# Kernel tuning notes

Measured on AMD Instinct MI355X. Metric: run time of the kernel, lower is better.

The kernel has to match this reference:

```python
import jax, jax.numpy as jnp
import numpy as np

NUM_EXPERTS = 8


def setup_inputs() -> dict:
    key = jax.random.key(0)
    k1, k2, k3, k4 = jax.random.split(key, 4)
    T, H, I, E = 1024, 1024, 4096, NUM_EXPERTS
    return {
        "hidden_states": jax.random.normal(k1, (T, H), dtype=jnp.float32),
        "w1": jax.random.normal(k2, (E, 2 * I, H), dtype=jnp.float32) * 0.02,
        "w2": jax.random.normal(k3, (E, H, I), dtype=jnp.float32) * 0.02,
        "gating_output": jax.random.normal(k4, (T, E), dtype=jnp.float32),
        "topk": 2,
    }


def reference(hidden_states, w1, w2, gating_output, topk):
    # Faithful single-device version of jax_fused_moe_func (renormalize=True,
    # reduce_results=True). The original sorts token copies by expert id and runs
    # a grouped matmul (megablox gmm), then reverts the sort; mathematically each
    # token copy is multiplied by its expert's weights, which we compute directly
    # (no sort/unsort permutation needed since it cancels).
    orig_shape = hidden_states.shape
    dtype = hidden_states.dtype
    H = hidden_states.shape[-1]
    T = hidden_states.size // H
    E = w1.shape[0]
    I = w2.shape[-1]  # intermediate_size

    hs = hidden_states.reshape(T, H)
    gates = gating_output.reshape(T, E)

    probs = jax.nn.softmax(gates.astype(jnp.float32), axis=-1)
    topk_weights, topk_indices = jax.lax.top_k(probs, k=topk)
    topk_weights = topk_weights / topk_weights.sum(axis=-1, keepdims=True)  # renormalize
    topk_weights = topk_weights.astype(dtype)

    flat_ids = topk_indices.reshape(-1)            # [T*topk] expert id per token copy
    x = jnp.repeat(hs, topk, axis=0)               # [T*topk, H] token copies

    out = jnp.zeros((T * topk, H), dtype=dtype)
    for e in range(E):  # fixed small expert loop (emulates grouped GEMM)
        h = x @ w1[e].T                            # [m, 2I]
        act = jax.nn.silu(h[:, :I]) * h[:, I:]     # SwiGLU
        y = act @ w2[e].T                          # [m, H]
        out = jnp.where((flat_ids == e)[:, None], y, out)

    out = (out.reshape(T, topk, H) * topk_weights[..., None]).sum(axis=-2)
    return out.reshape(orig_shape)
```

## Files before the change

kernel.cpp:

```cpp
#include <hip/hip_runtime.h>

#define T_TOK 1024
#define H_DIM 1024
#define I_DIM 4096
#define NE 8

typedef __attribute__((ext_vector_type(8))) short bf16x8;
typedef __attribute__((ext_vector_type(4))) float f32x4;
typedef __attribute__((ext_vector_type(8))) unsigned short us8;

__device__ __forceinline__ unsigned short f2bf(float x) {
  union { float f; unsigned u; } v; v.f = x;
  unsigned r = v.u + 0x7fffu + ((v.u >> 16) & 1u);
  return (unsigned short)(r >> 16);
}

__device__ __forceinline__ unsigned cvt_pk_bf16(float a, float b) {
  unsigned r;
  asm("v_cvt_pk_bf16_f32 %0, %1, %2" : "=v"(r) : "v"(a), "v"(b));
  return r;
}

__global__ void k_route(const float* __restrict__ gates, int* __restrict__ counts,
                        int* __restrict__ tok_idx, float* __restrict__ tok_w,
                        int* __restrict__ tok_cpy) {
  int t = blockIdx.x * blockDim.x + threadIdx.x;
  if (t >= T_TOK) return;
  float g[NE];
#pragma unroll
  for (int e = 0; e < NE; ++e) g[e] = gates[t * NE + e];
  int i1 = 0; float g1 = g[0];
#pragma unroll
  for (int e = 1; e < NE; ++e) if (g[e] > g1) { g1 = g[e]; i1 = e; }
  int i2 = -1; float g2 = -1e30f;
#pragma unroll
  for (int e = 0; e < NE; ++e) if (e != i1 && g[e] > g2) { g2 = g[e]; i2 = e; }
  float wa = 1.0f / (1.0f + expf(g2 - g1));
  float wb = 1.0f - wa;
  int s1 = atomicAdd(&counts[i1], 1);
  tok_idx[i1 * T_TOK + s1] = t; tok_w[i1 * T_TOK + s1] = wa; tok_cpy[i1 * T_TOK + s1] = 0;
  int s2 = atomicAdd(&counts[i2], 1);
  tok_idx[i2 * T_TOK + s2] = t; tok_w[i2 * T_TOK + s2] = wb; tok_cpy[i2 * T_TOK + s2] = 1;
}

__global__ void k_pack(const float* __restrict__ hs, const int* __restrict__ counts,
                       const int* __restrict__ tok_idx, const float* __restrict__ tok_w,
                       const int* __restrict__ tok_cpy, unsigned short* __restrict__ xpack,
                       int* __restrict__ row_tok, float* __restrict__ row_w,
                       int* __restrict__ inv_row) {
  int e = blockIdx.x >> 10, slot = blockIdx.x & 1023;
  if (slot >= counts[e]) return;
  int off = 0;
#pragma unroll
  for (int i = 0; i < NE; ++i) if (i < e) off += counts[i];
  int row = off + slot;
  int tok = tok_idx[e * T_TOK + slot];
  if (threadIdx.x == 0) {
    row_tok[row] = tok;
    row_w[row] = tok_w[e * T_TOK + slot];
    inv_row[tok * 2 + tok_cpy[e * T_TOK + slot]] = row;
  }
  float4 v = ((const float4*)(hs + (size_t)tok * H_DIM))[threadIdx.x];
  uint2 o; o.x = cvt_pk_bf16(v.x, v.y); o.y = cvt_pk_bf16(v.z, v.w);
  ((uint2*)(xpack + (size_t)row * H_DIM))[threadIdx.x] = o;
}

#define BK 64

__global__ __launch_bounds__(256)
void k_gemm1(const float* __restrict__ w1, const unsigned short* __restrict__ xpack,
             const int* __restrict__ counts, unsigned short* __restrict__ act) {
  int b = blockIdx.x;
  int x = b & 7, s = b >> 3;
  int mt = s & 7, pl = s >> 3;
  int panel = pl * 8 + x;
  int e = panel >> 6, ntile = panel & 63;
  int cnt = counts[e];
  int m0 = mt * 128;
  if (m0 >= cnt) return;
  int off = 0;
#pragma unroll
  for (int i = 0; i < NE; ++i) if (i < e) off += counts[i];
  int n0 = ntile * 64;

  __shared__ __align__(16) short As[128 * BK];
  __shared__ __align__(16) short Bs[128 * BK];

  int tid = threadIdx.x;
  int lane = tid & 63, wid = tid >> 6;
  int wm = wid & 1, wn = wid >> 1;
  int lr = lane & 15, lk8 = (lane >> 4) * 8;

  const float* w1e = w1 + (size_t)e * (2 * I_DIM) * H_DIM;
  const unsigned short* xb = xpack + (size_t)(off + m0) * H_DIM;

  int arow0 = tid >> 3, ack = tid & 7;
  int brow0 = tid >> 4, bck = tid & 15;

  const unsigned short* aptr[4];
  int awoff[4];
#pragma unroll
  for (int i = 0; i < 4; ++i) {
    int r = arow0 + i * 32;
    aptr[i] = xb + (size_t)r * H_DIM + ack * 8;
    awoff[i] = r * BK + ((ack * 8) ^ ((r & 7) << 3));
  }
  const float* bptr[8];
  int bwoff[8];
#pragma unroll
  for (int i = 0; i < 8; ++i) {
    int r = brow0 + i * 16;
    int grow = ((r & 16) ? I_DIM : 0) + n0 + ((r >> 5) << 4) + (r & 15);
    bptr[i] = w1e + (size_t)grow * H_DIM + bck * 4;
    bwoff[i] = r * BK + ((bck * 4) ^ ((r & 7) << 3));
  }

  f32x4 acc[4][4];
#pragma unroll
  for (int i = 0; i < 4; ++i)
#pragma unroll
    for (int j = 0; j < 4; ++j) acc[i][j] = (f32x4){0.f, 0.f, 0.f, 0.f};

  us8 aReg[4];
  float4 bReg[8];

  auto loadA = [&](int k0) {
#pragma unroll
    for (int i = 0; i < 4; ++i) {
      us8 z = {0, 0, 0, 0, 0, 0, 0, 0};
      aReg[i] = (m0 + arow0 + i * 32 < cnt) ? *(const us8*)(aptr[i] + k0) : z;
    }
  };
  auto loadB = [&](int k0) {
#pragma unroll
    for (int i = 0; i < 8; ++i) bReg[i] = *(const float4*)(bptr[i] + k0);
  };

  loadA(0); loadB(0);

  for (int ks = 0; ks < H_DIM / BK; ++ks) {
    __syncthreads();
#pragma unroll
    for (int i = 0; i < 4; ++i) *(us8*)&As[awoff[i]] = aReg[i];
#pragma unroll
    for (int i = 0; i < 8; ++i) {
      float4 v = bReg[i];
      uint2 o; o.x = cvt_pk_bf16(v.x, v.y); o.y = cvt_pk_bf16(v.z, v.w);
      *(uint2*)&Bs[bwoff[i]] = o;
    }
    __syncthreads();
    if (ks + 1 < H_DIM / BK) { loadA((ks + 1) * BK); loadB((ks + 1) * BK); }
#pragma unroll
    for (int kk = 0; kk < 2; ++kk) {
      int k0 = kk * 32 + lk8;
      bf16x8 a[4], bb[4];
#pragma unroll
      for (int mr = 0; mr < 4; ++mr) {
        int r = wm * 64 + mr * 16 + lr;
        a[mr] = *(const bf16x8*)&As[r * BK + (k0 ^ ((r & 7) << 3))];
      }
#pragma unroll
      for (int nr = 0; nr < 4; ++nr) {
        int r = wn * 64 + nr * 16 + lr;
        bb[nr] = *(const bf16x8*)&Bs[r * BK + (k0 ^ ((r & 7) << 3))];
      }
#pragma unroll
      for (int mr = 0; mr < 4; ++mr)
#pragma unroll
        for (int nr = 0; nr < 4; ++nr)
          acc[mr][nr] = __builtin_amdgcn_mfma_f32_16x16x32_bf16(a[mr], bb[nr], acc[mr][nr], 0, 0, 0);
    }
  }

#pragma unroll
  for (int mr = 0; mr < 4; ++mr) {
#pragma unroll
    for (int pp = 0; pp < 2; ++pp) {
      f32x4 g = acc[mr][2 * pp], u = acc[mr][2 * pp + 1];
      int ncol = n0 + (wn * 2 + pp) * 16 + lr;
#pragma unroll
      for (int q = 0; q < 4; ++q) {
        int rl = wm * 64 + mr * 16 + (lane >> 4) * 4 + q;
        if (m0 + rl < cnt) {
          float gv = g[q];
          float av = gv / (1.0f + expf(-gv)) * u[q];
          act[(size_t)(off + m0 + rl) * I_DIM + ncol] = f2bf(av);
        }
      }
    }
  }
}

__global__ __launch_bounds__(256)
void k_gemm2(const float* __restrict__ w2, const unsigned short* __restrict__ act,
             const int* __restrict__ counts, const float* __restrict__ row_w,
             float* __restrict__ y) {
  int b = blockIdx.x;
  int x = b & 7, s = b >> 3;
  int mt = s & 15, e = s >> 4;
  int ntile = x;
  int cnt = counts[e];
  int m0 = mt * 64;
  if (m0 >= cnt) return;
  int off = 0;
#pragma unroll
  for (int i = 0; i < NE; ++i) if (i < e) off += counts[i];
  int n0 = ntile * 128;

  __shared__ __align__(16) short As[64 * BK];
  __shared__ __align__(16) short Bs[128 * BK];

  int tid = threadIdx.x;
  int lane = tid & 63, wid = tid >> 6;
  int wm = wid & 1, wn = wid >> 1;
  int lr = lane & 15, lk8 = (lane >> 4) * 8;

  const float* w2e = w2 + (size_t)e * H_DIM * I_DIM;
  const unsigned short* ab = act + (size_t)(off + m0) * I_DIM;

  int arow0 = tid >> 3, ack = tid & 7;
  int brow0 = tid >> 4, bck = tid & 15;

  const unsigned short* aptr[2];
  int awoff[2];
#pragma unroll
  for (int i = 0; i < 2; ++i) {
    int r = arow0 + i * 32;
    aptr[i] = ab + (size_t)r * I_DIM + ack * 8;
    awoff[i] = r * BK + ((ack * 8) ^ ((r & 7) << 3));
  }
  const float* bptr[8];
  int bwoff[8];
#pragma unroll
  for (int i = 0; i < 8; ++i) {
    int r = brow0 + i * 16;
    bptr[i] = w2e + (size_t)(n0 + r) * I_DIM + bck * 4;
    bwoff[i] = r * BK + ((bck * 4) ^ ((r & 7) << 3));
  }

  f32x4 acc[2][4];
#pragma unroll
  for (int i = 0; i < 2; ++i)
#pragma unroll
    for (int j = 0; j < 4; ++j) acc[i][j] = (f32x4){0.f, 0.f, 0.f, 0.f};

  us8 aReg[2];
  float4 bReg[8];

  auto loadA = [&](int k0) {
#pragma unroll
    for (int i = 0; i < 2; ++i) {
      us8 z = {0, 0, 0, 0, 0, 0, 0, 0};
      aReg[i] = (m0 + arow0 + i * 32 < cnt) ? *(const us8*)(aptr[i] + k0) : z;
    }
  };
  auto loadB = [&](int k0) {
#pragma unroll
    for (int i = 0; i < 8; ++i) bReg[i] = *(const float4*)(bptr[i] + k0);
  };

  loadA(0); loadB(0);

  for (int ks = 0; ks < I_DIM / BK; ++ks) {
    __syncthreads();
#pragma unroll
    for (int i = 0; i < 2; ++i) *(us8*)&As[awoff[i]] = aReg[i];
#pragma unroll
    for (int i = 0; i < 8; ++i) {
      float4 v = bReg[i];
      uint2 o; o.x = cvt_pk_bf16(v.x, v.y); o.y = cvt_pk_bf16(v.z, v.w);
      *(uint2*)&Bs[bwoff[i]] = o;
    }
    __syncthreads();
    if (ks + 1 < I_DIM / BK) { loadA((ks + 1) * BK); loadB((ks + 1) * BK); }
#pragma unroll
    for (int kk = 0; kk < 2; ++kk) {
      int k0 = kk * 32 + lk8;
      bf16x8 a[2], bb[4];
#pragma unroll
      for (int mr = 0; mr < 2; ++mr) {
        int r = wm * 32 + mr * 16 + lr;
        a[mr] = *(const bf16x8*)&As[r * BK + (k0 ^ ((r & 7) << 3))];
      }
#pragma unroll
      for (int nr = 0; nr < 4; ++nr) {
        int r = (wn * 4 + nr) * 16 + lr;
        bb[nr] = *(const bf16x8*)&Bs[r * BK + (k0 ^ ((r & 7) << 3))];
      }
#pragma unroll
      for (int mr = 0; mr < 2; ++mr)
#pragma unroll
        for (int nr = 0; nr < 4; ++nr)
          acc[mr][nr] = __builtin_amdgcn_mfma_f32_16x16x32_bf16(a[mr], bb[nr], acc[mr][nr], 0, 0, 0);
    }
  }

#pragma unroll
  for (int mr = 0; mr < 2; ++mr) {
#pragma unroll
    for (int q = 0; q < 4; ++q) {
      int rl = wm * 32 + mr * 16 + (lane >> 4) * 4 + q;
      if (m0 + rl >= cnt) continue;
      int grow = off + m0 + rl;
      float wgt = row_w[grow];
      float* yrow = y + (size_t)grow * H_DIM;
#pragma unroll
      for (int nr = 0; nr < 4; ++nr) {
        int ncol = n0 + (wn * 4 + nr) * 16 + lr;
        yrow[ncol] = acc[mr][nr][q] * wgt;
      }
    }
  }
}

__global__ void k_combine(const float* __restrict__ y, const int* __restrict__ inv_row,
                          float* __restrict__ out) {
  int t = blockIdx.x, i = threadIdx.x;
  const float4* ya = (const float4*)(y + (size_t)inv_row[2 * t] * H_DIM);
  const float4* yb = (const float4*)(y + (size_t)inv_row[2 * t + 1] * H_DIM);
  float4 a = ya[i], b2 = yb[i];
  ((float4*)(out + (size_t)t * H_DIM))[i] =
      make_float4(a.x + b2.x, a.y + b2.y, a.z + b2.z, a.w + b2.w);
}

extern "C" void kernel_launch(void* const* d_in, const int* in_sizes, int n_in,
                              void* d_out, int out_size, void* d_ws, size_t ws_size,
                              hipStream_t stream) {
  const float* hs = (const float*)d_in[0];
  const float* w1 = (const float*)d_in[1];
  const float* w2 = (const float*)d_in[2];
  const float* gates = (const float*)d_in[3];
  float* out = (float*)d_out;

  char* ws = (char*)d_ws;
  int* counts = (int*)ws;
  int* tok_idx = (int*)(ws + 4096);
  float* tok_w = (float*)(ws + 4096 + 32768);
  int* tok_cpy = (int*)(ws + 4096 + 65536);
  int* row_tok = (int*)(ws + 4096 + 98304);
  float* row_w = (float*)(ws + 4096 + 98304 + 8192);
  int* inv_row = (int*)(ws + 4096 + 98304 + 16384);
  unsigned short* xpack = (unsigned short*)(ws + (1 << 17));
  unsigned short* act = (unsigned short*)(ws + (8u << 20));
  float* y = (float*)(ws + (32u << 20));

  hipMemsetAsync(counts, 0, NE * sizeof(int), stream);
  k_route<<<dim3(4), dim3(256), 0, stream>>>(gates, counts, tok_idx, tok_w, tok_cpy);
  k_pack<<<dim3(NE * T_TOK), dim3(256), 0, stream>>>(hs, counts, tok_idx, tok_w, tok_cpy,
                                                     xpack, row_tok, row_w, inv_row);
  k_gemm1<<<dim3(4096), dim3(256), 0, stream>>>(w1, xpack, counts, act);
  k_gemm2<<<dim3(1024), dim3(256), 0, stream>>>(w2, act, counts, row_w, y);
  k_combine<<<dim3(T_TOK), dim3(256), 0, stream>>>(y, inv_row, out);
}
```

Measured before the change: 258.2 us.

## Shrink GEMM tiles and split GEMM2 K four ways for more parallel blocks

GEMM1 N-tiles are halved (64 to 32 columns per gate/up pair), doubling the grid. GEMM2 uses 64-wide N tiles and splits the K=4096 reduction into four chunks that write separate partial outputs. The combine kernel then sums the four partials for both token copies. This targets low occupancy from only a few active blocks per expert, at the cost of re-reading A tiles more often, less MFMA work per LDS load, and extra partial-buffer traffic in the combine step. The unused row_tok buffer is also dropped.

```diff
diff --git a/kernel.cpp b/kernel.cpp
--- a/kernel.cpp
+++ b/kernel.cpp
@@ -46,8 +46,7 @@
 __global__ void k_pack(const float* __restrict__ hs, const int* __restrict__ counts,
                        const int* __restrict__ tok_idx, const float* __restrict__ tok_w,
                        const int* __restrict__ tok_cpy, unsigned short* __restrict__ xpack,
-                       int* __restrict__ row_tok, float* __restrict__ row_w,
-                       int* __restrict__ inv_row) {
+                       float* __restrict__ row_w, int* __restrict__ inv_row) {
   int e = blockIdx.x >> 10, slot = blockIdx.x & 1023;
   if (slot >= counts[e]) return;
   int off = 0;
@@ -56,7 +55,6 @@
   int row = off + slot;
   int tok = tok_idx[e * T_TOK + slot];
   if (threadIdx.x == 0) {
-    row_tok[row] = tok;
     row_w[row] = tok_w[e * T_TOK + slot];
     inv_row[tok * 2 + tok_cpy[e * T_TOK + slot]] = row;
   }
@@ -74,17 +72,17 @@
   int x = b & 7, s = b >> 3;
   int mt = s & 7, pl = s >> 3;
   int panel = pl * 8 + x;
-  int e = panel >> 6, ntile = panel & 63;
+  int e = panel >> 7, ntile = panel & 127;
   int cnt = counts[e];
   int m0 = mt * 128;
   if (m0 >= cnt) return;
   int off = 0;
 #pragma unroll
   for (int i = 0; i < NE; ++i) if (i < e) off += counts[i];
-  int n0 = ntile * 64;
+  int n0 = ntile * 32;
 
   __shared__ __align__(16) short As[128 * BK];
-  __shared__ __align__(16) short Bs[128 * BK];
+  __shared__ __align__(16) short Bs[64 * BK];
 
   int tid = threadIdx.x;
   int lane = tid & 63, wid = tid >> 6;
@@ -105,24 +103,24 @@
     aptr[i] = xb + (size_t)r * H_DIM + ack * 8;
     awoff[i] = r * BK + ((ack * 8) ^ ((r & 7) << 3));
   }
-  const float* bptr[8];
-  int bwoff[8];
-#pragma unroll
-  for (int i = 0; i < 8; ++i) {
+  const float* bptr[4];
+  int bwoff[4];
+#pragma unroll
+  for (int i = 0; i < 4; ++i) {
     int r = brow0 + i * 16;
     int grow = ((r & 16) ? I_DIM : 0) + n0 + ((r >> 5) << 4) + (r & 15);
     bptr[i] = w1e + (size_t)grow * H_DIM + bck * 4;
     bwoff[i] = r * BK + ((bck * 4) ^ ((r & 7) << 3));
   }
 
-  f32x4 acc[4][4];
+  f32x4 acc[4][2];
 #pragma unroll
   for (int i = 0; i < 4; ++i)
 #pragma unroll
-    for (int j = 0; j < 4; ++j) acc[i][j] = (f32x4){0.f, 0.f, 0.f, 0.f};
+    for (int j = 0; j < 2; ++j) acc[i][j] = (f32x4){0.f, 0.f, 0.f, 0.f};
 
   us8 aReg[4];
-  float4 bReg[8];
+  float4 bReg[4];
 
   auto loadA = [&](int k0) {
 #pragma unroll
@@ -133,7 +131,7 @@
   };
   auto loadB = [&](int k0) {
 #pragma unroll
-    for (int i = 0; i < 8; ++i) bReg[i] = *(const float4*)(bptr[i] + k0);
+    for (int i = 0; i < 4; ++i) bReg[i] = *(const float4*)(bptr[i] + k0);
   };
 
   loadA(0); loadB(0);
@@ -143,7 +141,7 @@
 #pragma unroll
     for (int i = 0; i < 4; ++i) *(us8*)&As[awoff[i]] = aReg[i];
 #pragma unroll
-    for (int i = 0; i < 8; ++i) {
+    for (int i = 0; i < 4; ++i) {
       float4 v = bReg[i];
       uint2 o; o.x = cvt_pk_bf16(v.x, v.y); o.y = cvt_pk_bf16(v.z, v.w);
       *(uint2*)&Bs[bwoff[i]] = o;
@@ -153,39 +151,36 @@
 #pragma unroll
     for (int kk = 0; kk < 2; ++kk) {
       int k0 = kk * 32 + lk8;
-      bf16x8 a[4], bb[4];
+      bf16x8 a[4], bb[2];
 #pragma unroll
       for (int mr = 0; mr < 4; ++mr) {
         int r = wm * 64 + mr * 16 + lr;
         a[mr] = *(const bf16x8*)&As[r * BK + (k0 ^ ((r & 7) << 3))];
       }
 #pragma unroll
-      for (int nr = 0; nr < 4; ++nr) {
-        int r = wn * 64 + nr * 16 + lr;
+      for (int nr = 0; nr < 2; ++nr) {
+        int r = (wn * 2 + nr) * 16 + lr;
         bb[nr] = *(const bf16x8*)&Bs[r * BK + (k0 ^ ((r & 7) << 3))];
       }
 #pragma unroll
       for (int mr = 0; mr < 4; ++mr)
 #pragma unroll
-        for (int nr = 0; nr < 4; ++nr)
+        for (int nr = 0; nr < 2; ++nr)
           acc[mr][nr] = __builtin_amdgcn_mfma_f32_16x16x32_bf16(a[mr], bb[nr], acc[mr][nr], 0, 0, 0);
     }
   }
 
 #pragma unroll
   for (int mr = 0; mr < 4; ++mr) {
-#pragma unroll
-    for (int pp = 0; pp < 2; ++pp) {
-      f32x4 g = acc[mr][2 * pp], u = acc[mr][2 * pp + 1];
-      int ncol = n0 + (wn * 2 + pp) * 16 + lr;
-#pragma unroll
-      for (int q = 0; q < 4; ++q) {
-        int rl = wm * 64 + mr * 16 + (lane >> 4) * 4 + q;
-        if (m0 + rl < cnt) {
-          float gv = g[q];
-          float av = gv / (1.0f + expf(-gv)) * u[q];
-          act[(size_t)(off + m0 + rl) * I_DIM + ncol] = f2bf(av);
-        }
+    f32x4 g = acc[mr][0], u = acc[mr][1];
+    int ncol = n0 + wn * 16 + lr;
+#pragma unroll
+    for (int q = 0; q < 4; ++q) {
+      int rl = wm * 64 + mr * 16 + (lane >> 4) * 4 + q;
+      if (m0 + rl < cnt) {
+        float gv = g[q];
+        float av = gv / (1.0f + expf(-gv)) * u[q];
+        act[(size_t)(off + m0 + rl) * I_DIM + ncol] = f2bf(av);
       }
     }
   }
@@ -194,21 +189,24 @@
 __global__ __launch_bounds__(256)
 void k_gemm2(const float* __restrict__ w2, const unsigned short* __restrict__ act,
              const int* __restrict__ counts, const float* __restrict__ row_w,
-             float* __restrict__ y) {
+             float* __restrict__ yp) {
   int b = blockIdx.x;
   int x = b & 7, s = b >> 3;
-  int mt = s & 15, e = s >> 4;
-  int ntile = x;
+  int mt = s & 15, pl = s >> 4;
+  int panel = pl * 8 + x;
+  int e = panel >> 6;
+  int nt = (panel & 63) >> 2, kc = panel & 3;
   int cnt = counts[e];
   int m0 = mt * 64;
   if (m0 >= cnt) return;
   int off = 0;
 #pragma unroll
   for (int i = 0; i < NE; ++i) if (i < e) off += counts[i];
-  int n0 = ntile * 128;
+  int n0 = nt * 64;
+  int kbase = kc * 1024;
 
   __shared__ __align__(16) short As[64 * BK];
-  __shared__ __align__(16) short Bs[128 * BK];
+  __shared__ __align__(16) short Bs[64 * BK];
 
   int tid = threadIdx.x;
   int lane = tid & 63, wid = tid >> 6;
@@ -226,26 +224,26 @@
 #pragma unroll
   for (int i = 0; i < 2; ++i) {
     int r = arow0 + i * 32;
-    aptr[i] = ab + (size_t)r * I_DIM + ack * 8;
+    aptr[i] = ab + (size_t)r * I_DIM + kbase + ack * 8;
     awoff[i] = r * BK + ((ack * 8) ^ ((r & 7) << 3));
   }
-  const float* bptr[8];
-  int bwoff[8];
-#pragma unroll
-  for (int i = 0; i < 8; ++i) {
+  const float* bptr[4];
+  int bwoff[4];
+#pragma unroll
+  for (int i = 0; i < 4; ++i) {
     int r = brow0 + i * 16;
-    bptr[i] = w2e + (size_t)(n0 + r) * I_DIM + bck * 4;
+    bptr[i] = w2e + (size_t)(n0 + r) * I_DIM + kbase + bck * 4;
     bwoff[i] = r * BK + ((bck * 4) ^ ((r & 7) << 3));
   }
 
-  f32x4 acc[2][4];
+  f32x4 acc[2][2];
 #pragma unroll
   for (int i = 0; i < 2; ++i)
 #pragma unroll
-    for (int j = 0; j < 4; ++j) acc[i][j] = (f32x4){0.f, 0.f, 0.f, 0.f};
+    for (int j = 0; j < 2; ++j) acc[i][j] = (f32x4){0.f, 0.f, 0.f, 0.f};
 
   us8 aReg[2];
-  float4 bReg[8];
+  float4 bReg[4];
 
   auto loadA = [&](int k0) {
 #pragma unroll
@@ -256,45 +254,46 @@
   };
   auto loadB = [&](int k0) {
 #pragma unroll
-    for (int i = 0; i < 8; ++i) bReg[i] = *(const float4*)(bptr[i] + k0);
+    for (int i = 0; i < 4; ++i) bReg[i] = *(const float4*)(bptr[i] + k0);
   };
 
   loadA(0); loadB(0);
 
-  for (int ks = 0; ks < I_DIM / BK; ++ks) {
+  for (int ks = 0; ks < 1024 / BK; ++ks) {
     __syncthreads();
 #pragma unroll
     for (int i = 0; i < 2; ++i) *(us8*)&As[awoff[i]] = aReg[i];
 #pragma unroll
-    for (int i = 0; i < 8; ++i) {
+    for (int i = 0; i < 4; ++i) {
       float4 v = bReg[i];
       uint2 o; o.x = cvt_pk_bf16(v.x, v.y); o.y = cvt_pk_bf16(v.z, v.w);
       *(uint2*)&Bs[bwoff[i]] = o;
     }
     __syncthreads();
-    if (ks + 1 < I_DIM / BK) { loadA((ks + 1) * BK); loadB((ks + 1) * BK); }
+    if (ks + 1 < 1024 / BK) { loadA((ks + 1) * BK); loadB((ks + 1) * BK); }
 #pragma unroll
     for (int kk = 0; kk < 2; ++kk) {
       int k0 = kk * 32 + lk8;
-      bf16x8 a[2], bb[4];
+      bf16x8 a[2], bb[2];
 #pragma unroll
       for (int mr = 0; mr < 2; ++mr) {
         int r = wm * 32 + mr * 16 + lr;
         a[mr] = *(const bf16x8*)&As[r * BK + (k0 ^ ((r & 7) << 3))];
       }
 #pragma unroll
-      for (int nr = 0; nr < 4; ++nr) {
-        int r = (wn * 4 + nr) * 16 + lr;
+      for (int nr = 0; nr < 2; ++nr) {
+        int r = wn * 32 + nr * 16 + lr;
         bb[nr] = *(const bf16x8*)&Bs[r * BK + (k0 ^ ((r & 7) << 3))];
       }
 #pragma unroll
       for (int mr = 0; mr < 2; ++mr)
 #pragma unroll
-        for (int nr = 0; nr < 4; ++nr)
+        for (int nr = 0; nr < 2; ++nr)
           acc[mr][nr] = __builtin_amdgcn_mfma_f32_16x16x32_bf16(a[mr], bb[nr], acc[mr][nr], 0, 0, 0);
     }
   }
 
+  float* ypc = yp + (size_t)kc * (2048 * H_DIM);
 #pragma unroll
   for (int mr = 0; mr < 2; ++mr) {
 #pragma unroll
@@ -303,24 +302,29 @@
       if (m0 + rl >= cnt) continue;
       int grow = off + m0 + rl;
       float wgt = row_w[grow];
-      float* yrow = y + (size_t)grow * H_DIM;
-#pragma unroll
-      for (int nr = 0; nr < 4; ++nr) {
-        int ncol = n0 + (wn * 4 + nr) * 16 + lr;
+      float* yrow = ypc + (size_t)grow * H_DIM;
+#pragma unroll
+      for (int nr = 0; nr < 2; ++nr) {
+        int ncol = n0 + wn * 32 + nr * 16 + lr;
         yrow[ncol] = acc[mr][nr][q] * wgt;
       }
     }
   }
 }
 
-__global__ void k_combine(const float* __restrict__ y, const int* __restrict__ inv_row,
+__global__ void k_combine(const float* __restrict__ yp, const int* __restrict__ inv_row,
                           float* __restrict__ out) {
   int t = blockIdx.x, i = threadIdx.x;
-  const float4* ya = (const float4*)(y + (size_t)inv_row[2 * t] * H_DIM);
-  const float4* yb = (const float4*)(y + (size_t)inv_row[2 * t + 1] * H_DIM);
-  float4 a = ya[i], b2 = yb[i];
-  ((float4*)(out + (size_t)t * H_DIM))[i] =
-      make_float4(a.x + b2.x, a.y + b2.y, a.z + b2.z, a.w + b2.w);
+  int r0 = inv_row[2 * t], r1 = inv_row[2 * t + 1];
+  float4 s = make_float4(0.f, 0.f, 0.f, 0.f);
+#pragma unroll
+  for (int kc = 0; kc < 4; ++kc) {
+    const float4* a = (const float4*)(yp + (size_t)kc * (2048 * H_DIM) + (size_t)r0 * H_DIM);
+    const float4* b = (const float4*)(yp + (size_t)kc * (2048 * H_DIM) + (size_t)r1 * H_DIM);
+    float4 va = a[i], vb = b[i];
+    s.x += va.x + vb.x; s.y += va.y + vb.y; s.z += va.z + vb.z; s.w += va.w + vb.w;
+  }
+  ((float4*)(out + (size_t)t * H_DIM))[i] = s;
 }
 
 extern "C" void kernel_launch(void* const* d_in, const int* in_sizes, int n_in,
@@ -337,18 +341,17 @@
   int* tok_idx = (int*)(ws + 4096);
   float* tok_w = (float*)(ws + 4096 + 32768);
   int* tok_cpy = (int*)(ws + 4096 + 65536);
-  int* row_tok = (int*)(ws + 4096 + 98304);
-  float* row_w = (float*)(ws + 4096 + 98304 + 8192);
-  int* inv_row = (int*)(ws + 4096 + 98304 + 16384);
+  float* row_w = (float*)(ws + 4096 + 98304);
+  int* inv_row = (int*)(ws + 4096 + 98304 + 8192);
   unsigned short* xpack = (unsigned short*)(ws + (1 << 17));
   unsigned short* act = (unsigned short*)(ws + (8u << 20));
-  float* y = (float*)(ws + (32u << 20));
+  float* yp = (float*)(ws + (32u << 20));
 
   hipMemsetAsync(counts, 0, NE * sizeof(int), stream);
   k_route<<<dim3(4), dim3(256), 0, stream>>>(gates, counts, tok_idx, tok_w, tok_cpy);
   k_pack<<<dim3(NE * T_TOK), dim3(256), 0, stream>>>(hs, counts, tok_idx, tok_w, tok_cpy,
-                                                     xpack, row_tok, row_w, inv_row);
-  k_gemm1<<<dim3(4096), dim3(256), 0, stream>>>(w1, xpack, counts, act);
-  k_gemm2<<<dim3(1024), dim3(256), 0, stream>>>(w2, act, counts, row_w, y);
-  k_combine<<<dim3(T_TOK), dim3(256), 0, stream>>>(y, inv_row, out);
-}
+                                                     xpack, row_w, inv_row);
+  k_gemm1<<<dim3(8192), dim3(256), 0, stream>>>(w1, xpack, counts, act);
+  k_gemm2<<<dim3(8192), dim3(256), 0, stream>>>(w2, act, counts, row_w, yp);
+  k_combine<<<dim3(T_TOK), dim3(256), 0, stream>>>(yp, inv_row, out);
+}
```

Result: faster. 222.1 us (-14.0%).
